# Kernel tuning notes

Hardware: AMD Instinct MI355X
Metric: run time of the kernel (lower is better)

## Reference

```python
import jax, jax.numpy as jnp
import numpy as np

NUM_HEADS = 12
EMB = 768
HEAD = 64
SEQ = 2048
BATCH = 2


def setup_inputs() -> dict:
    key = jax.random.key(0)
    ks = jax.random.split(key, 6)
    scale = 0.02
    x = jax.random.normal(ks[0], (BATCH, SEQ, EMB), dtype=jnp.float32)
    # per-head Q/K/V projections (bias-free, Karpathy-style HeadAttention), batched over heads
    Wq = jax.random.normal(ks[1], (NUM_HEADS, EMB, HEAD), dtype=jnp.float32) * scale
    Wk = jax.random.normal(ks[2], (NUM_HEADS, EMB, HEAD), dtype=jnp.float32) * scale
    Wv = jax.random.normal(ks[3], (NUM_HEADS, EMB, HEAD), dtype=jnp.float32) * scale
    # output projection: Linear(head_size*num_heads, emb_size)
    Wo = jax.random.normal(ks[4], (NUM_HEADS * HEAD, EMB), dtype=jnp.float32) * scale
    bo = jax.random.normal(ks[5], (EMB,), dtype=jnp.float32) * scale
    return {"x": x, "Wq": Wq, "Wk": Wk, "Wv": Wv, "Wo": Wo, "bo": bo}


def reference(x, Wq, Wk, Wv, Wo, bo):
    B, S, E = x.shape
    # batched per-head projections: [B,S,E] x [H,E,D] -> [B,H,S,D]
    q = jnp.einsum("bse,hed->bhsd", x, Wq)
    k = jnp.einsum("bse,hed->bhsd", x, Wk)
    v = jnp.einsum("bse,hed->bhsd", x, Wv)
    scale = 1.0 / jnp.sqrt(jnp.asarray(HEAD, dtype=x.dtype))
    scores = jnp.einsum("bhsd,bhtd->bhst", q, k) * scale  # [B,H,S,S]
    causal = jnp.tril(jnp.ones((S, S), dtype=bool))
    scores = jnp.where(causal, scores, jnp.asarray(-jnp.inf, dtype=scores.dtype))
    attn = jax.nn.softmax(scores, axis=-1)
    out = jnp.einsum("bhst,bhtd->bhsd", attn, v)  # [B,H,S,D]
    # concat heads along last dim: [B,S,H*D]
    out = out.transpose(0, 2, 1, 3).reshape(B, S, NUM_HEADS * HEAD)
    # output projection (dropout is identity in eval mode)
    return out @ Wo + bo
```

## Files before the change

kernel.cpp:

```cpp
#include <hip/hip_runtime.h>

#define NHEAD 12
#define EMB 768
#define HDD 64
#define SEQ 2048

typedef __attribute__((ext_vector_type(4))) float f32x4;
typedef __attribute__((ext_vector_type(8))) short short8;
typedef __attribute__((ext_vector_type(4))) short short4v;
typedef unsigned int u32;

#define GLL16(g, l)                                                            \
    __builtin_amdgcn_global_load_lds(                                          \
        (const __attribute__((address_space(1))) u32*)(g),                     \
        (__attribute__((address_space(3))) u32*)(l), 16, 0, 0)

static __device__ __forceinline__ short bf16s(float f) {
    unsigned u = __builtin_bit_cast(unsigned, f);
    u = (u + 0x7fffu + ((u >> 16) & 1u)) >> 16;
    return (short)u;
}

__global__ void k_cvt_all(const float* __restrict__ x, const float* __restrict__ Wq,
                          const float* __restrict__ Wk, const float* __restrict__ Wv,
                          const float* __restrict__ Wo, short* __restrict__ xb,
                          short* __restrict__ WqT, short* __restrict__ WkT,
                          short* __restrict__ WvT, short* __restrict__ WoT) {
    const int bid = blockIdx.x, t = threadIdx.x;
    if (bid < 1536) {
        const int i = (bid * 256 + t) * 8;
        const f32x4* s = (const f32x4*)(x + i);
        f32x4 a = s[0], b = s[1];
        short8 o;
        o[0] = bf16s(a[0]); o[1] = bf16s(a[1]); o[2] = bf16s(a[2]); o[3] = bf16s(a[3]);
        o[4] = bf16s(b[0]); o[5] = bf16s(b[1]); o[6] = bf16s(b[2]); o[7] = bf16s(b[3]);
        *(short8*)(xb + i) = o;
    } else if (bid < 1968) {
        const int idx = bid - 1536;
        const int h = idx % 12, e0 = ((idx / 12) % 12) * 64, z = idx / 144;
        const float* W = z == 0 ? Wq : (z == 1 ? Wk : Wv);
        short* Wt = z == 0 ? WqT : (z == 1 ? WkT : WvT);
        __shared__ float tile[64][65];
        const int r = t >> 2, c0 = (t & 3) * 16;
        const float* src = W + (h * EMB + e0 + r) * HDD + c0;
#pragma unroll
        for (int i = 0; i < 16; ++i) tile[r][c0 + i] = src[i];
        __syncthreads();
        short* dst = Wt + (h * HDD + r) * EMB + e0 + c0;
#pragma unroll
        for (int i = 0; i < 16; ++i) dst[i] = bf16s(tile[c0 + i][r]);
    } else {
        const int idx = bid - 1968;
        const int k0 = (idx % 12) * 64, n0 = (idx / 12) * 64;
        __shared__ float tile[64][65];
        const int r = t >> 2, c0 = (t & 3) * 16;
        const float* src = Wo + (k0 + r) * EMB + n0 + c0;
#pragma unroll
        for (int i = 0; i < 16; ++i) tile[r][c0 + i] = src[i];
        __syncthreads();
        short* dst = WoT + (n0 + r) * EMB + k0 + c0;
#pragma unroll
        for (int i = 0; i < 16; ++i) dst[i] = bf16s(tile[c0 + i][r]);
    }
}

template <int MODE>
__global__ __launch_bounds__(256) void k_gemm(
        const short* __restrict__ xb, const short* __restrict__ Wt0,
        const short* __restrict__ Wt1, const short* __restrict__ Wt2,
        short* __restrict__ Qo, short* __restrict__ Ko, short* __restrict__ Vo,
        const float* __restrict__ bias, float* __restrict__ Fout) {
    __shared__ alignas(16) short As[128 * 32];
    __shared__ alignas(16) short Bs[128 * 32];
    const int t = threadIdx.x, lane = t & 63, wave = t >> 6;
    const int z = (MODE == 0) ? blockIdx.z : 0;
    const short* Ap;
    const short* Bp;
    int m0, n0;
    if (MODE == 1) {
        Ap = xb; Bp = Wt0; m0 = blockIdx.y * 128; n0 = blockIdx.x * 128;
    } else if (z == 0) {
        Ap = xb; Bp = Wt0; m0 = blockIdx.y * 128; n0 = blockIdx.x * 128;
    } else if (z == 1) {
        Ap = xb; Bp = Wt1; m0 = blockIdx.y * 128; n0 = blockIdx.x * 128;
    } else {
        Ap = Wt2; Bp = xb; m0 = blockIdx.x * 128; n0 = blockIdx.y * 128;
    }

    const int srow = lane >> 2;
    const int scolSw = ((lane & 3) ^ ((srow >> 1) & 3)) * 8;
    const short* gA = Ap + (long)(m0 + wave * 32 + srow) * EMB + scolSw;
    const short* gB = Bp + (long)(n0 + wave * 32 + srow) * EMB + scolSw;
    short* lA = As + (wave * 32) * 32;
    short* lB = Bs + (wave * 32) * 32;

    const int wm = (wave >> 1) * 64, wn = (wave & 1) * 64;
    const int fr = lane & 15, hi = lane >> 4;
    const int rdoff = (hi ^ ((fr >> 1) & 3)) * 8;

    f32x4 acc[4][4];
#pragma unroll
    for (int i = 0; i < 4; ++i)
#pragma unroll
        for (int j = 0; j < 4; ++j)
#pragma unroll
            for (int e = 0; e < 4; ++e) acc[i][j][e] = 0.f;

    for (int kk = 0; kk < EMB; kk += 32) {
        __syncthreads();
        GLL16(gA + kk, lA);
        GLL16(gA + kk + 16 * EMB, lA + 16 * 32);
        GLL16(gB + kk, lB);
        GLL16(gB + kk + 16 * EMB, lB + 16 * 32);
        __syncthreads();
        short8 af[4], bfq[4];
#pragma unroll
        for (int i = 0; i < 4; ++i)
            af[i] = *(const short8*)(As + (wm + i * 16 + fr) * 32 + rdoff);
#pragma unroll
        for (int j = 0; j < 4; ++j)
            bfq[j] = *(const short8*)(Bs + (wn + j * 16 + fr) * 32 + rdoff);
#pragma unroll
        for (int i = 0; i < 4; ++i)
#pragma unroll
            for (int j = 0; j < 4; ++j)
                acc[i][j] = __builtin_amdgcn_mfma_f32_16x16x32_bf16(af[i], bfq[j], acc[i][j], 0, 0, 0);
    }

    const int r0 = hi * 4;
#pragma unroll
    for (int i = 0; i < 4; ++i) {
#pragma unroll
        for (int j = 0; j < 4; ++j) {
            const int nbase = n0 + wn + j * 16 + fr;
            float bj = 0.f;
            if (MODE == 1) bj = bias[nbase];
#pragma unroll
            for (int r = 0; r < 4; ++r) {
                const int m = m0 + wm + i * 16 + r0 + r;
                float v = acc[i][j][r];
                if (MODE == 0) {
                    if (z == 2) {
                        const int hh = m >> 6, dd = m & 63;
                        const int bb = nbase >> 11, ss = nbase & 2047;
                        Vo[(long)((bb * NHEAD + hh) * HDD + dd) * SEQ + ss] = bf16s(v);
                    } else {
                        const int bb = m >> 11, ss = m & 2047;
                        const int hh = nbase >> 6, dd = nbase & 63;
                        short* Dst = (z == 0) ? Qo : Ko;
                        if (z == 0) v *= 0.125f;
                        Dst[(long)((bb * NHEAD + hh) * SEQ + ss) * HDD + dd] = bf16s(v);
                    }
                } else {
                    Fout[(long)m * EMB + nbase] = v + bj;
                }
            }
        }
    }
}

__global__ __launch_bounds__(256) void k_attn(
        const short* __restrict__ Q, const short* __restrict__ K,
        const short* __restrict__ VT, short* __restrict__ O) {
    __shared__ alignas(16) short Kbuf[2][64 * 72];
    __shared__ alignas(16) short Vbuf[2][64 * 72];
    __shared__ alignas(16) short Ps[4][16 * 72];
    const int bh = blockIdx.x;
    const int h = bh % NHEAD, b = bh / NHEAD;
    const int qs = (int)gridDim.y - 1 - (int)blockIdx.y;
    const int q0 = qs * 64;
    const int ntile = qs + 1;
    const int t = threadIdx.x, lane = t & 63, wave = t >> 6;
    const long base = (long)(b * NHEAD + h) * SEQ * HDD;
    const short* Qg = Q + base;
    const short* Kg = K + base;
    const short* Vg = VT + base;
    const int fr = lane & 15, hi = lane >> 4, fk = hi * 8, r0 = hi * 4;
    const int wq = q0 + wave * 16;

    short8 qf[2];
#pragma unroll
    for (int c = 0; c < 2; ++c)
        qf[c] = *(const short8*)(Qg + (long)(wq + fr) * HDD + c * 32 + fk);

    f32x4 oacc[4];
#pragma unroll
    for (int i = 0; i < 4; ++i)
#pragma unroll
        for (int e = 0; e < 4; ++e) oacc[i][e] = 0.f;
    float mrun = -3e38f, lrun = 0.f;

    const int srow = t >> 2, sc = (t & 3) * 16;
    const short* KgS = Kg + (long)srow * HDD + sc;
    const short* VgS = Vg + (long)srow * SEQ + sc;
    short* Pw = &Ps[wave][0];

    short8 kv0 = *(const short8*)(KgS);
    short8 kv1 = *(const short8*)(KgS + 8);
    short8 vv0 = *(const short8*)(VgS);
    short8 vv1 = *(const short8*)(VgS + 8);
    *(short8*)(&Kbuf[0][srow * 72 + sc]) = kv0;
    *(short8*)(&Kbuf[0][srow * 72 + sc + 8]) = kv1;
    *(short8*)(&Vbuf[0][srow * 72 + sc]) = vv0;
    *(short8*)(&Vbuf[0][srow * 72 + sc + 8]) = vv1;
    if (ntile > 1) {
        kv0 = *(const short8*)(KgS + (long)64 * HDD);
        kv1 = *(const short8*)(KgS + (long)64 * HDD + 8);
        vv0 = *(const short8*)(VgS + 64);
        vv1 = *(const short8*)(VgS + 64 + 8);
    }
    __syncthreads();

    for (int kt = 0; kt < ntile; ++kt) {
        const int k0 = kt * 64;
        const int cur = kt & 1;
        if (kt + 1 < ntile) {
            *(short8*)(&Kbuf[cur ^ 1][srow * 72 + sc]) = kv0;
            *(short8*)(&Kbuf[cur ^ 1][srow * 72 + sc + 8]) = kv1;
            *(short8*)(&Vbuf[cur ^ 1][srow * 72 + sc]) = vv0;
            *(short8*)(&Vbuf[cur ^ 1][srow * 72 + sc + 8]) = vv1;
            if (kt + 2 < ntile) {
                kv0 = *(const short8*)(KgS + (long)(k0 + 128) * HDD);
                kv1 = *(const short8*)(KgS + (long)(k0 + 128) * HDD + 8);
                vv0 = *(const short8*)(VgS + (k0 + 128));
                vv1 = *(const short8*)(VgS + (k0 + 128) + 8);
            }
        }
        if (k0 <= wq + 15) {
            const short* Ks = &Kbuf[cur][0];
            const short* Vs = &Vbuf[cur][0];

            f32x4 st[4];
#pragma unroll
            for (int nt = 0; nt < 4; ++nt) {
                const short8 kf0 = *(const short8*)(Ks + (nt * 16 + fr) * 72 + fk);
                const short8 kf1 = *(const short8*)(Ks + (nt * 16 + fr) * 72 + 32 + fk);
#pragma unroll
                for (int e = 0; e < 4; ++e) st[nt][e] = 0.f;
                st[nt] = __builtin_amdgcn_mfma_f32_16x16x32_bf16(kf0, qf[0], st[nt], 0, 0, 0);
                st[nt] = __builtin_amdgcn_mfma_f32_16x16x32_bf16(kf1, qf[1], st[nt], 0, 0, 0);
            }

            float p[4][4];
            float pmax = -3e38f;
            if (k0 + 63 > wq) {
                const int myq = wq + fr;
#pragma unroll
                for (int nt = 0; nt < 4; ++nt)
#pragma unroll
                    for (int r = 0; r < 4; ++r) {
                        float s = st[nt][r];
                        if (k0 + nt * 16 + r0 + r > myq) s = -3e38f;
                        p[nt][r] = s;
                        pmax = fmaxf(pmax, s);
                    }
            } else {
#pragma unroll
                for (int nt = 0; nt < 4; ++nt)
#pragma unroll
                    for (int r = 0; r < 4; ++r) {
                        p[nt][r] = st[nt][r];
                        pmax = fmaxf(pmax, st[nt][r]);
                    }
            }
            pmax = fmaxf(pmax, __shfl_xor(pmax, 16, 64));
            pmax = fmaxf(pmax, __shfl_xor(pmax, 32, 64));
            const float mnew = fmaxf(mrun, pmax);
            const float corr = __expf(mrun - mnew);
            mrun = mnew;
            float rsum = 0.f;
#pragma unroll
            for (int nt = 0; nt < 4; ++nt)
#pragma unroll
                for (int r = 0; r < 4; ++r) {
                    const float e = __expf(p[nt][r] - mnew);
                    p[nt][r] = e;
                    rsum += e;
                }
            rsum += __shfl_xor(rsum, 16, 64);
            rsum += __shfl_xor(rsum, 32, 64);
            lrun = lrun * corr + rsum;
#pragma unroll
            for (int dt = 0; dt < 4; ++dt)
#pragma unroll
                for (int e = 0; e < 4; ++e) oacc[dt][e] *= corr;

#pragma unroll
            for (int nt = 0; nt < 4; ++nt) {
                short4v pk;
                pk[0] = bf16s(p[nt][0]);
                pk[1] = bf16s(p[nt][1]);
                pk[2] = bf16s(p[nt][2]);
                pk[3] = bf16s(p[nt][3]);
                *(short4v*)(Pw + fr * 72 + nt * 16 + r0) = pk;
            }

#pragma unroll
            for (int kc = 0; kc < 2; ++kc) {
                const short8 pf = *(const short8*)(Pw + fr * 72 + kc * 32 + fk);
#pragma unroll
                for (int dt = 0; dt < 4; ++dt) {
                    const short8 vf = *(const short8*)(Vs + (dt * 16 + fr) * 72 + kc * 32 + fk);
                    oacc[dt] = __builtin_amdgcn_mfma_f32_16x16x32_bf16(vf, pf, oacc[dt], 0, 0, 0);
                }
            }
        }
        __syncthreads();
    }

    short* Os = &Ps[0][0];
    const float iv = 1.0f / lrun;
#pragma unroll
    for (int dt = 0; dt < 4; ++dt)
#pragma unroll
        for (int r = 0; r < 4; ++r)
            Os[(wave * 16 + fr) * 72 + dt * 16 + r0 + r] = bf16s(oacc[dt][r] * iv);
    __syncthreads();
    {
        const int row = t >> 2, c0 = (t & 3) * 16;
        const short8 o0 = *(const short8*)(Os + row * 72 + c0);
        const short8 o1 = *(const short8*)(Os + row * 72 + c0 + 8);
        short* Og = O + (long)(b * SEQ + q0 + row) * EMB + h * HDD + c0;
        *(short8*)Og = o0;
        *(short8*)(Og + 8) = o1;
    }
}

extern "C" void kernel_launch(void* const* d_in, const int* in_sizes, int n_in,
                              void* d_out, int out_size, void* d_ws, size_t ws_size,
                              hipStream_t stream) {
    const float* x  = (const float*)d_in[0];
    const float* Wq = (const float*)d_in[1];
    const float* Wk = (const float*)d_in[2];
    const float* Wv = (const float*)d_in[3];
    const float* Wo = (const float*)d_in[4];
    const float* bo = (const float*)d_in[5];
    float* out = (float*)d_out;

    char* ws = (char*)d_ws;
    short* xb  = (short*)(ws + 0);
    short* WqT = (short*)(ws + 6291456);
    short* WkT = (short*)(ws + 7471104);
    short* WvT = (short*)(ws + 8650752);
    short* WoT = (short*)(ws + 9830400);
    short* Qb  = (short*)(ws + 11010048);
    short* Kb  = (short*)(ws + 17301504);
    short* VTb = (short*)(ws + 23592960);
    short* Ob  = (short*)(ws + 29884416);

    k_cvt_all<<<dim3(2112), dim3(256), 0, stream>>>(
        x, Wq, Wk, Wv, Wo, xb, WqT, WkT, WvT, WoT);
    k_gemm<0><<<dim3(6, 32, 3), dim3(256), 0, stream>>>(
        xb, WqT, WkT, WvT, Qb, Kb, VTb, (const float*)nullptr, (float*)nullptr);
    k_attn<<<dim3(24, 32), dim3(256), 0, stream>>>(Qb, Kb, VTb, Ob);
    k_gemm<1><<<dim3(6, 32, 1), dim3(256), 0, stream>>>(
        Ob, WoT, (const short*)nullptr, (const short*)nullptr,
        (short*)nullptr, (short*)nullptr, (short*)nullptr, bo, out);
}
```

Baseline: 100.1 us.

## Split long causal query tiles across two KV chunks with merge kernel

Query tiles 16-31 are split into two KV-range chunks, each computed by a separate block that writes unnormalized partial outputs plus running max and sum. A new merge kernel combines the two partials with the usual log-sum-exp rescaling. The aim is to balance the causal triangular workload and shorten the longest blocks. In exchange it adds an extra kernel launch, partial-output traffic through workspace, and bf16 rounding of the unnormalized partials.

```diff
diff --git a/kernel.cpp b/kernel.cpp
--- a/kernel.cpp
+++ b/kernel.cpp
@@ -19,6 +19,10 @@
     unsigned u = __builtin_bit_cast(unsigned, f);
     u = (u + 0x7fffu + ((u >> 16) & 1u)) >> 16;
     return (short)u;
+}
+static __device__ __forceinline__ float bf2f(short s) {
+    unsigned u = ((unsigned)(unsigned short)s) << 16;
+    return __builtin_bit_cast(float, u);
 }
 
 __global__ void k_cvt_all(const float* __restrict__ x, const float* __restrict__ Wq,
@@ -161,15 +165,19 @@
 
 __global__ __launch_bounds__(256) void k_attn(
         const short* __restrict__ Q, const short* __restrict__ K,
-        const short* __restrict__ VT, short* __restrict__ O) {
+        const short* __restrict__ VT, short* __restrict__ O,
+        short* __restrict__ Ub, float* __restrict__ Mb, float* __restrict__ Lb) {
     __shared__ alignas(16) short Kbuf[2][64 * 72];
     __shared__ alignas(16) short Vbuf[2][64 * 72];
     __shared__ alignas(16) short Ps[4][16 * 72];
     const int bh = blockIdx.x;
     const int h = bh % NHEAD, b = bh / NHEAD;
-    const int qs = (int)gridDim.y - 1 - (int)blockIdx.y;
+    const int yy = blockIdx.y;
+    int qs, kb, ke, chunk, split;
+    if (yy < 16)      { qs = 16 + yy; kb = 0;  ke = 16;     chunk = 0; split = 1; }
+    else if (yy < 32) { qs = yy;      kb = 16; ke = qs + 1; chunk = 1; split = 1; }
+    else              { qs = 47 - yy; kb = 0;  ke = qs + 1; chunk = 0; split = 0; }
     const int q0 = qs * 64;
-    const int ntile = qs + 1;
     const int t = threadIdx.x, lane = t & 63, wave = t >> 6;
     const long base = (long)(b * NHEAD + h) * SEQ * HDD;
     const short* Qg = Q + base;
@@ -195,31 +203,31 @@
     const short* VgS = Vg + (long)srow * SEQ + sc;
     short* Pw = &Ps[wave][0];
 
-    short8 kv0 = *(const short8*)(KgS);
-    short8 kv1 = *(const short8*)(KgS + 8);
-    short8 vv0 = *(const short8*)(VgS);
-    short8 vv1 = *(const short8*)(VgS + 8);
+    short8 kv0 = *(const short8*)(KgS + (long)(kb * 64) * HDD);
+    short8 kv1 = *(const short8*)(KgS + (long)(kb * 64) * HDD + 8);
+    short8 vv0 = *(const short8*)(VgS + kb * 64);
+    short8 vv1 = *(const short8*)(VgS + kb * 64 + 8);
     *(short8*)(&Kbuf[0][srow * 72 + sc]) = kv0;
     *(short8*)(&Kbuf[0][srow * 72 + sc + 8]) = kv1;
     *(short8*)(&Vbuf[0][srow * 72 + sc]) = vv0;
     *(short8*)(&Vbuf[0][srow * 72 + sc + 8]) = vv1;
-    if (ntile > 1) {
-        kv0 = *(const short8*)(KgS + (long)64 * HDD);
-        kv1 = *(const short8*)(KgS + (long)64 * HDD + 8);
-        vv0 = *(const short8*)(VgS + 64);
-        vv1 = *(const short8*)(VgS + 64 + 8);
+    if (ke - kb > 1) {
+        kv0 = *(const short8*)(KgS + (long)(kb * 64 + 64) * HDD);
+        kv1 = *(const short8*)(KgS + (long)(kb * 64 + 64) * HDD + 8);
+        vv0 = *(const short8*)(VgS + kb * 64 + 64);
+        vv1 = *(const short8*)(VgS + kb * 64 + 64 + 8);
     }
     __syncthreads();
 
-    for (int kt = 0; kt < ntile; ++kt) {
+    for (int kt = kb; kt < ke; ++kt) {
         const int k0 = kt * 64;
-        const int cur = kt & 1;
-        if (kt + 1 < ntile) {
+        const int cur = (kt - kb) & 1;
+        if (kt + 1 < ke) {
             *(short8*)(&Kbuf[cur ^ 1][srow * 72 + sc]) = kv0;
             *(short8*)(&Kbuf[cur ^ 1][srow * 72 + sc + 8]) = kv1;
             *(short8*)(&Vbuf[cur ^ 1][srow * 72 + sc]) = vv0;
             *(short8*)(&Vbuf[cur ^ 1][srow * 72 + sc + 8]) = vv1;
-            if (kt + 2 < ntile) {
+            if (kt + 2 < ke) {
                 kv0 = *(const short8*)(KgS + (long)(k0 + 128) * HDD);
                 kv1 = *(const short8*)(KgS + (long)(k0 + 128) * HDD + 8);
                 vv0 = *(const short8*)(VgS + (k0 + 128));
@@ -306,6 +314,21 @@
             }
         }
         __syncthreads();
+    }
+
+    if (split) {
+        const int pidx = (bh * 16 + (qs - 16)) * 2 + chunk;
+        short* Up = Ub + pidx * 4096;
+#pragma unroll
+        for (int dt = 0; dt < 4; ++dt)
+#pragma unroll
+            for (int r = 0; r < 4; ++r)
+                Up[(dt * 16 + r0 + r) * 64 + wave * 16 + fr] = bf16s(oacc[dt][r]);
+        if (lane < 16) {
+            Mb[pidx * 64 + wave * 16 + lane] = mrun;
+            Lb[pidx * 64 + wave * 16 + lane] = lrun;
+        }
+        return;
     }
 
     short* Os = &Ps[0][0];
@@ -326,6 +349,55 @@
     }
 }
 
+__global__ __launch_bounds__(256) void k_merge(
+        const short* __restrict__ Ub, const float* __restrict__ Mb,
+        const float* __restrict__ Lb, short* __restrict__ O) {
+    __shared__ float aS[64], bS[64], iL[64];
+    __shared__ short tile[64 * 72];
+    const int bid = blockIdx.x;
+    const int bh = bid >> 4, sidx = bid & 15;
+    const int h = bh % NHEAD, b = bh / NHEAD;
+    const int q0 = (16 + sidx) * 64;
+    const int p0 = (bh * 16 + sidx) * 2, p1 = p0 + 1;
+    const int t = threadIdx.x;
+    if (t < 64) {
+        const float m1 = Mb[p0 * 64 + t], m2 = Mb[p1 * 64 + t];
+        const float l1 = Lb[p0 * 64 + t], l2 = Lb[p1 * 64 + t];
+        const float m = fmaxf(m1, m2);
+        const float a = __expf(m1 - m), bb = __expf(m2 - m);
+        aS[t] = a;
+        bS[t] = bb;
+        iL[t] = 1.0f / (l1 * a + l2 * bb);
+    }
+    __syncthreads();
+    {
+        const int d = t >> 2, qg = (t & 3) * 16;
+        const short8 u1a = *(const short8*)(Ub + p0 * 4096 + d * 64 + qg);
+        const short8 u1b = *(const short8*)(Ub + p0 * 4096 + d * 64 + qg + 8);
+        const short8 u2a = *(const short8*)(Ub + p1 * 4096 + d * 64 + qg);
+        const short8 u2b = *(const short8*)(Ub + p1 * 4096 + d * 64 + qg + 8);
+#pragma unroll
+        for (int i = 0; i < 8; ++i) {
+            const int q = qg + i;
+            tile[q * 72 + d] = bf16s((bf2f(u1a[i]) * aS[q] + bf2f(u2a[i]) * bS[q]) * iL[q]);
+        }
+#pragma unroll
+        for (int i = 0; i < 8; ++i) {
+            const int q = qg + 8 + i;
+            tile[q * 72 + d] = bf16s((bf2f(u1b[i]) * aS[q] + bf2f(u2b[i]) * bS[q]) * iL[q]);
+        }
+    }
+    __syncthreads();
+    {
+        const int q = t >> 2, dg = (t & 3) * 16;
+        const short8 o0 = *(const short8*)(tile + q * 72 + dg);
+        const short8 o1 = *(const short8*)(tile + q * 72 + dg + 8);
+        short* Og = O + (long)(b * SEQ + q0 + q) * EMB + h * HDD + dg;
+        *(short8*)Og = o0;
+        *(short8*)(Og + 8) = o1;
+    }
+}
+
 extern "C" void kernel_launch(void* const* d_in, const int* in_sizes, int n_in,
                               void* d_out, int out_size, void* d_ws, size_t ws_size,
                               hipStream_t stream) {
@@ -347,12 +419,16 @@
     short* Kb  = (short*)(ws + 17301504);
     short* VTb = (short*)(ws + 23592960);
     short* Ob  = (short*)(ws + 29884416);
+    short* Ub  = (short*)(ws + 0);
+    float* Mb  = (float*)(ws + 6291456);
+    float* Lb  = (float*)(ws + 6488064);
 
     k_cvt_all<<<dim3(2112), dim3(256), 0, stream>>>(
         x, Wq, Wk, Wv, Wo, xb, WqT, WkT, WvT, WoT);
     k_gemm<0><<<dim3(6, 32, 3), dim3(256), 0, stream>>>(
         xb, WqT, WkT, WvT, Qb, Kb, VTb, (const float*)nullptr, (float*)nullptr);
-    k_attn<<<dim3(24, 32), dim3(256), 0, stream>>>(Qb, Kb, VTb, Ob);
+    k_attn<<<dim3(24, 48), dim3(256), 0, stream>>>(Qb, Kb, VTb, Ob, Ub, Mb, Lb);
+    k_merge<<<dim3(384), dim3(256), 0, stream>>>(Ub, Mb, Lb, Ob);
     k_gemm<1><<<dim3(6, 32, 1), dim3(256), 0, stream>>>(
         Ob, WoT, (const short*)nullptr, (const short*)nullptr,
         (short*)nullptr, (short*)nullptr, (short*)nullptr, bo, out);
```

After: 95.71 us. -4.4%, faster.
